# Kernel optimization log

Hardware: AMD Instinct MI355X
Metric: run time of the kernel (lower is better)

## Reference

```python
import jax, jax.numpy as jnp
from jax import lax
import numpy as np

EPS = 1e-5
NH = 16  # attention heads (c // 16 with c = 256)


def _qconv(x, mod, phase, padding=0, groups=1):
    """Quaternion conv: real weight = modulus * cos(phase), applied per quaternion component.
    x: (B, C, Q, H, W) -> (B, O, Q, H, W)"""
    w = mod * jnp.cos(phase)
    B, C, Qd, H, W = x.shape
    xr = jnp.transpose(x, (0, 2, 1, 3, 4)).reshape(B * Qd, C, H, W)
    y = lax.conv_general_dilated(xr, w, (1, 1), [(padding, padding)] * 2,
                                 dimension_numbers=('NCHW', 'OIHW', 'NCHW'),
                                 feature_group_count=groups)
    O, Ho, Wo = y.shape[1], y.shape[2], y.shape[3]
    return jnp.transpose(y.reshape(B, Qd, O, Ho, Wo), (0, 2, 1, 3, 4))


def _bn(x):
    # IQBN/VQBN: per-channel normalization over (batch, quaternion, spatial), no affine
    m = x.mean(axis=(0, 2, 3, 4), keepdims=True)
    v = x.var(axis=(0, 2, 3, 4), keepdims=True)
    return (x - m) * lax.rsqrt(v + EPS)


def _attn(x, qkv_m, qkv_p, aproj_m, aproj_p, pe_m, pe_p):
    # QAttention: per-component multi-head self-attention over spatial tokens
    B, C, Qd, H, W = x.shape
    kd = C // NH
    qkv = _qconv(x, qkv_m, qkv_p)  # (B, 3C, Q, H, W)
    q, k, v = jnp.split(qkv, 3, axis=1)
    q = q.reshape(B, NH, kd, Qd, H * W)
    k = k.reshape(B, NH, kd, Qd, H * W)
    v = v.reshape(B, NH, kd, Qd, H * W)
    scores = jnp.einsum('bhcqn,bhcqm->bhqnm', q, k) * (kd ** -0.5)
    a = jax.nn.softmax(scores, axis=-1)
    out = jnp.einsum('bhqnm,bhdqm->bhdqn', a, v).reshape(B, C, Qd, H, W)
    # proj + depthwise positional conv on the input
    return _qconv(out, aproj_m, aproj_p) + _qconv(x, pe_m, pe_p, padding=1, groups=C)


def _psa(x, qkv_m, qkv_p, aproj_m, aproj_p, pe_m, pe_p, ffn1_m, ffn1_p, ffn2_m, ffn2_p):
    a = _attn(x, qkv_m, qkv_p, aproj_m, aproj_p, pe_m, pe_p) + x  # attn shortcut
    h = jax.nn.relu(_bn(_qconv(a, ffn1_m, ffn1_p)))
    f = _bn(_qconv(h, ffn2_m, ffn2_p))
    return f + a  # ffn shortcut


def _msab(x, guide, ec_m, ec_p, gl_w, gl_b, mproj_m, mproj_p):
    # MaxSigmoidAttnBlock (nh=1): global sigmoid gate per (batch, quaternion component)
    B, C, Qd, H, W = x.shape
    e = jax.nn.relu(_bn(_qconv(x, ec_m, ec_p)))  # (B, ec, Q, H, W)
    g = guide @ gl_w.T + gl_b                     # (B, ec)
    ec = g.shape[-1]
    a = jnp.einsum('bcqhw,bc->bq', e, g) / jnp.sqrt(jnp.asarray(ec * H * W, jnp.float32))
    a = jax.nn.sigmoid(a)  # scale param = 1.0 (scale=False)
    e = e * a[:, None, :, None, None]
    return jax.nn.relu(_bn(_qconv(e, mproj_m, mproj_p, padding=1)))


def _forward(x, guide, cv1_m, cv1_p, qkv_m, qkv_p, aproj_m, aproj_p, pe_m, pe_p,
             ffn1_m, ffn1_p, ffn2_m, ffn2_p, ec_m, ec_p, gl_w, gl_b,
             mproj_m, mproj_p, cv2_m, cv2_p):
    y = jax.nn.relu(_bn(_qconv(x, cv1_m, cv1_p)))       # (B, 2c, Q, H, W)
    a, b = jnp.split(y, 2, axis=1)                       # each (B, c, Q, H, W)
    p = _psa(b, qkv_m, qkv_p, aproj_m, aproj_p, pe_m, pe_p,
             ffn1_m, ffn1_p, ffn2_m, ffn2_p)
    m = _msab(p, guide, ec_m, ec_p, gl_w, gl_b, mproj_m, mproj_p)
    cat = jnp.concatenate([a, b, p, m], axis=1)          # (B, 4c, Q, H, W)
    return jax.nn.relu(_bn(_qconv(cat, cv2_m, cv2_p)))   # (B, c2, Q, H, W)


def setup_inputs():
    B, C1, Qd, H, W = 2, 512, 4, 24, 24
    c = 256; ecd = 128; gc = 512; C2 = 512
    ks = jax.random.split(jax.random.key(0), 24)
    def rp(k, shape, s=0.02):
        return s * jax.random.normal(k, shape, dtype=jnp.float32)
    return {
        'x': jax.random.normal(ks[0], (B, C1, Qd, H, W), dtype=jnp.float32),
        'guide': jax.random.normal(ks[1], (B, gc), dtype=jnp.float32),
        'cv1_m': rp(ks[2], (2 * c, C1, 1, 1)),
        'cv1_p': rp(ks[3], (2 * c, C1, 1, 1), 0.1),
        'qkv_m': rp(ks[4], (3 * c, c, 1, 1)),
        'qkv_p': rp(ks[5], (3 * c, c, 1, 1), 0.1),
        'aproj_m': rp(ks[6], (c, c, 1, 1)),
        'aproj_p': rp(ks[7], (c, c, 1, 1), 0.1),
        'pe_m': rp(ks[8], (c, 1, 3, 3)),
        'pe_p': rp(ks[9], (c, 1, 3, 3), 0.1),
        'ffn1_m': rp(ks[10], (2 * c, c, 1, 1)),
        'ffn1_p': rp(ks[11], (2 * c, c, 1, 1), 0.1),
        'ffn2_m': rp(ks[12], (c, 2 * c, 1, 1)),
        'ffn2_p': rp(ks[13], (c, 2 * c, 1, 1), 0.1),
        'ec_m': rp(ks[14], (ecd, c, 1, 1)),
        'ec_p': rp(ks[15], (ecd, c, 1, 1), 0.1),
        'gl_w': rp(ks[16], (ecd, gc), 0.05),
        'gl_b': jnp.zeros((ecd,), dtype=jnp.float32),
        'mproj_m': rp(ks[17], (c, ecd, 3, 3)),
        'mproj_p': rp(ks[18], (c, ecd, 3, 3), 0.1),
        'cv2_m': rp(ks[19], (C2, 4 * c, 1, 1)),
        'cv2_p': rp(ks[20], (C2, 4 * c, 1, 1), 0.1),
    }


def reference(x, guide, cv1_m, cv1_p, qkv_m, qkv_p, aproj_m, aproj_p, pe_m, pe_p,
              ffn1_m, ffn1_p, ffn2_m, ffn2_p, ec_m, ec_p, gl_w, gl_b,
              mproj_m, mproj_p, cv2_m, cv2_p):
    return _forward(x, guide, cv1_m, cv1_p, qkv_m, qkv_p, aproj_m, aproj_p, pe_m, pe_p,
                    ffn1_m, ffn1_p, ffn2_m, ffn2_p, ec_m, ec_p, gl_w, gl_b,
                    mproj_m, mproj_p, cv2_m, cv2_p)
```

## Files before the change

kernel.cpp:

```cpp
#include <hip/hip_runtime.h>
#include <math.h>

typedef __bf16 bf16x8 __attribute__((ext_vector_type(8)));
typedef float f32x4 __attribute__((ext_vector_type(4)));
typedef unsigned short u16;
typedef unsigned int u32;

__device__ __forceinline__ u16 f2bf(float f) {
  u32 u = __float_as_uint(f);
  u32 r = u + 0x7FFF + ((u >> 16) & 1);
  return (u16)(r >> 16);
}
__device__ __forceinline__ float bf2f(u16 h) { return __uint_as_float(((u32)h) << 16); }

static constexpr size_t OB_WBF = 0;
static constexpr size_t OB_WPE = 3276800;
static constexpr size_t OB_ST  = 3286016;
static constexpr size_t OB_GV  = 3310592;
static constexpr size_t OB_GACC= 3311616;
static constexpr size_t OB_CAT = 3311872;
static constexpr size_t OB_YA  = OB_CAT + 9437184;
static constexpr size_t OB_U1  = OB_YA + 9437184;
static constexpr size_t OB_U2  = OB_U1 + 4718592;
static constexpr size_t OB_U3  = OB_U2 + 14155776;
static constexpr size_t OB_AOB = OB_U3 + 4718592;
static constexpr size_t OB_A1B = OB_AOB + 2359296;
static constexpr size_t WS_TOTAL = OB_A1B + 2359296;

struct HeadP {
  const float* m[8]; const float* p[8]; u16* wout;
  const float* pem; const float* pep; float* peout;
  const float* x; u16* xb;
  const float* guide; const float* glw; const float* glb; float* gv;
  int cum[9]; int nwp;
};
__global__ __launch_bounds__(256) void k_head(HeadP P) {
  int bid = blockIdx.x;
  if (bid < P.nwp) {
    int i = bid * 256 + threadIdx.x;
    if (i < 2304) {
      int tap = i >> 8, c = i & 255;
      P.peout[i] = P.pem[c * 9 + tap] * cosf(P.pep[c * 9 + tap]);
    }
    if (i >= P.cum[8]) return;
    int s = 0;
    while (s < 7 && i >= P.cum[s + 1]) s++;
    int j = i - P.cum[s];
    int src = j;
    if (s == 6) {
      int o = j / 1152, r = j % 1152, kk = r >> 7, cc = r & 127;
      src = (o * 128 + cc) * 9 + kk;
    }
    P.wout[i] = f2bf(P.m[s][src] * cosf(P.p[s][src]));
    return;
  }
  bid -= P.nwp;
  if (bid < 2304) {
    int mt = bid % 18; bid /= 18;
    int ct = bid % 16; bid /= 16;
    int q = bid & 3, b = bid >> 2;
    __shared__ float tile[32][33];
    int tj = threadIdx.x & 31, ti = threadIdx.x >> 5;
    const float* xp = P.x + (((size_t)(b * 512 + ct * 32) * 4 + q) * 576) + mt * 32;
#pragma unroll
    for (int ii = 0; ii < 4; ii++)
      tile[ti + ii * 8][tj] = xp[(size_t)(ti + ii * 8) * 4 * 576 + tj];
    __syncthreads();
    u16* yp = P.xb + ((size_t)b * 2304 + q * 576 + mt * 32) * 512 + ct * 32;
#pragma unroll
    for (int mm = 0; mm < 4; mm++)
      yp[(size_t)(mm * 8 + ti) * 512 + tj] = f2bf(tile[tj][mm * 8 + ti]);
    return;
  }
  bid -= 2304;
  int wv = threadIdx.x >> 6, lane = threadIdx.x & 63;
  int be = bid * 4 + wv;
  int b = be >> 7, e = be & 127;
  const float* gr = P.guide + b * 512;
  const float* wr = P.glw + e * 512;
  float s = 0.f;
  for (int c = lane; c < 512; c += 64) s = fmaf(gr[c], wr[c], s);
#pragma unroll
  for (int off = 32; off > 0; off >>= 1) s += __shfl_down(s, off, 64);
  if (lane == 0) P.gv[be] = s + P.glb[e];
}

struct GemmP {
  const u16* W; const u16* X; float* Y; u16* Yb; float* St;
  const u16* CAT; const float* W9;
  const float* EF; const float* GA;
  long long xOff[8];
  int lda, O, K, M, G;
};

template <int BM, int NWO, int WO, int WM, int MODE>
__global__ __launch_bounds__(256) void k_gemm(GemmP P) {
  constexpr int FO = WO / 16, FM = WM / 16;
  __shared__ __align__(16) char lds[16384 + BM * 128];
  const int mt = P.M / BM;
  const int ot = P.O >> 7;
  int bid = blockIdx.x;
  const int g = bid / (mt * ot);
  const int rr = bid % (mt * ot);
  const int ob = (rr / mt) << 7;
  const int mb = (rr % mt) * BM;
  const int t = threadIdx.x, lane = t & 63, wave = t >> 6;
  const int wo = (wave % NWO) * WO, wm = (wave / NWO) * WM;
  const u16* Wp = P.W + (size_t)ob * P.K;
  const u16* Xp = (MODE == 2) ? nullptr : (P.X + P.xOff[g] + (size_t)mb * P.lda);

  float gt = 0.f;
  int bq2304 = 0;
  if constexpr (MODE == 2) {
    bq2304 = (g >> 2) * 2304 + (g & 3) * 576;
    float a = P.GA[g] / sqrtf(73728.0f);
    gt = 1.f / (1.f + __expf(-a));
  }

  f32x4 acc[FO][FM] = {};

  for (int k0 = 0; k0 < P.K; k0 += 64) {
#pragma unroll
    for (int i = 0; i < 4; i++) {
      int s = (i * 4 + wave) * 64 + lane;
      int row = s >> 3;
      int kg = (s & 7) ^ (row & 7);
      const u16* src = Wp + (size_t)row * P.K + k0 + kg * 8;
      __builtin_amdgcn_global_load_lds(
          (const __attribute__((address_space(1))) u32*)src,
          (__attribute__((address_space(3))) u32*)(lds + (size_t)(i * 4 + wave) * 1024),
          16, 0, 0);
    }
    if constexpr (MODE != 2) {
#pragma unroll
      for (int i = 0; i < BM * 8 / 256; i++) {
        int s = (i * 4 + wave) * 64 + lane;
        int row = s >> 3;
        int kg = (s & 7) ^ (row & 7);
        const u16* src = Xp + (size_t)row * P.lda + k0 + kg * 8;
        __builtin_amdgcn_global_load_lds(
            (const __attribute__((address_space(1))) u32*)src,
            (__attribute__((address_space(3))) u32*)(lds + 16384 + (size_t)(i * 4 + wave) * 1024),
            16, 0, 0);
      }
    } else {
#pragma unroll
      for (int i = 0; i < 2; i++) {
        int s = t + i * 256;
        int row = s >> 3, kg = s & 7;
        int k = k0 + kg * 8;
        int kk = k >> 7, cc = k & 127;
        int n = mb + row;
        int h = n / 24 + kk / 3 - 1, w = n % 24 + kk % 3 - 1;
        u16 pk[8];
        if (h >= 0 && h < 24 && w >= 0 && w < 24) {
          const float* ep = P.EF + ((size_t)(bq2304 + h * 24 + w)) * 128 + cc;
          f32x4 v0 = *(const f32x4*)ep;
          f32x4 v1 = *(const f32x4*)(ep + 4);
#pragma unroll
          for (int j = 0; j < 4; j++) {
            pk[j] = f2bf(v0[j] * gt);
            pk[4 + j] = f2bf(v1[j] * gt);
          }
        } else {
#pragma unroll
          for (int j = 0; j < 8; j++) pk[j] = 0;
        }
        *(uint4*)&lds[16384 + (((row << 3) + (kg ^ (row & 7))) << 4)] = *(uint4*)pk;
      }
    }
    __syncthreads();
#pragma unroll
    for (int kk = 0; kk < 2; kk++) {
      int kgl = kk * 4 + (lane >> 4);
      bf16x8 af[FO], bfm[FM];
#pragma unroll
      for (int fo = 0; fo < FO; fo++) {
        int row = wo + fo * 16 + (lane & 15);
        af[fo] = *(bf16x8*)&lds[((row << 3) + (kgl ^ (row & 7))) << 4];
      }
#pragma unroll
      for (int fm = 0; fm < FM; fm++) {
        int row = wm + fm * 16 + (lane & 15);
        bfm[fm] = *(bf16x8*)&lds[16384 + (((row << 3) + (kgl ^ (row & 7))) << 4)];
      }
#pragma unroll
      for (int fo = 0; fo < FO; fo++)
#pragma unroll
        for (int fm = 0; fm < FM; fm++)
          acc[fo][fm] = __builtin_amdgcn_mfma_f32_16x16x32_bf16(af[fo], bfm[fm], acc[fo][fm], 0, 0, 0);
    }
    __syncthreads();
  }

  size_t ybase = (size_t)g * P.M * P.O;
#pragma unroll
  for (int fo = 0; fo < FO; fo++) {
    int ow = ob + wo + fo * 16 + ((lane >> 4) << 2);
#pragma unroll
    for (int fm = 0; fm < FM; fm++) {
      int m = mb + wm + fm * 16 + (lane & 15);
      f32x4 v = acc[fo][fm];
      if constexpr (MODE == 1) {
        size_t tokc = ((size_t)g * 2304 + m) * 1024 + 256 + ow;
        ushort4 cv = *(const ushort4*)&P.CAT[tokc];
        v[0] += bf2f(cv.x); v[1] += bf2f(cv.y); v[2] += bf2f(cv.z); v[3] += bf2f(cv.w);
        int q_ = m / 576, hw_ = m % 576, h_ = hw_ / 24, w_ = hw_ % 24;
        size_t rowb = ((size_t)g * 2304 + q_ * 576) * 1024 + 256 + ow;
#pragma unroll
        for (int tp = 0; tp < 9; tp++) {
          int hh = h_ + tp / 3 - 1, ww = w_ + tp % 3 - 1;
          if (hh < 0 || hh > 23 || ww < 0 || ww > 23) continue;
          ushort4 tv = *(const ushort4*)&P.CAT[rowb + (size_t)(hh * 24 + ww) * 1024];
          f32x4 wt = *(const f32x4*)&P.W9[tp * 256 + ow];
          v[0] = fmaf(wt[0], bf2f(tv.x), v[0]);
          v[1] = fmaf(wt[1], bf2f(tv.y), v[1]);
          v[2] = fmaf(wt[2], bf2f(tv.z), v[2]);
          v[3] = fmaf(wt[3], bf2f(tv.w), v[3]);
        }
        acc[fo][fm] = v;
      }
      size_t off = ybase + (size_t)m * P.O + ow;
      if (P.Y) *(f32x4*)&P.Y[off] = v;
      if (P.Yb) {
        ushort4 r;
        r.x = f2bf(v[0]); r.y = f2bf(v[1]); r.z = f2bf(v[2]); r.w = f2bf(v[3]);
        *(ushort4*)&P.Yb[off] = r;
      }
    }
  }

  if (P.St) {
#pragma unroll
    for (int fo = 0; fo < FO; fo++) {
      float sv[4], qv[4];
#pragma unroll
      for (int j = 0; j < 4; j++) { sv[j] = 0.f; qv[j] = 0.f; }
#pragma unroll
      for (int fm = 0; fm < FM; fm++)
#pragma unroll
        for (int j = 0; j < 4; j++) {
          float a = acc[fo][fm][j];
          sv[j] += a;
          qv[j] = fmaf(a, a, qv[j]);
        }
#pragma unroll
      for (int j = 0; j < 4; j++) {
#pragma unroll
        for (int mk = 1; mk < 16; mk <<= 1) {
          sv[j] += __shfl_xor(sv[j], mk, 64);
          qv[j] += __shfl_xor(qv[j], mk, 64);
        }
      }
      if ((lane & 15) == 0) {
        int o = ob + wo + fo * 16 + ((lane >> 4) << 2);
#pragma unroll
        for (int j = 0; j < 4; j++) {
          atomicAdd(&P.St[2 * (o + j)], sv[j]);
          atomicAdd(&P.St[2 * (o + j) + 1], qv[j]);
        }
      }
    }
  }
}

struct NormP {
  const float* X; const float* st; const u16* AddB;
  u16* Yb; float* Yf; const float* gv; float* gacc;
  long long ybOff[8];
  int ldyb, O, G, M, relu;
  float n;
};
__global__ __launch_bounds__(256) void k_norm(NormP P) {
  int O4 = P.O >> 2;
  long long idx = (long long)blockIdx.x * 256 + threadIdx.x;
  if (idx >= (long long)P.G * P.M * O4) return;
  int c4 = (int)(idx % O4);
  long long gm = idx / O4;
  int m = (int)(gm % P.M);
  int g = (int)(gm / P.M);
  size_t off = (size_t)gm * P.O + c4 * 4;
  f32x4 v = *(const f32x4*)&P.X[off];
  float inv_n = 1.0f / P.n;
#pragma unroll
  for (int j = 0; j < 4; j++) {
    int c = c4 * 4 + j;
    float mean = P.st[2 * c] * inv_n;
    float var = P.st[2 * c + 1] * inv_n - mean * mean;
    v[j] = (v[j] - mean) * rsqrtf(var + 1e-5f);
  }
  if (P.AddB) {
    ushort4 av = *(const ushort4*)(P.AddB + off);
    v[0] += bf2f(av.x); v[1] += bf2f(av.y); v[2] += bf2f(av.z); v[3] += bf2f(av.w);
  }
  if (P.relu) {
#pragma unroll
    for (int j = 0; j < 4; j++) v[j] = fmaxf(v[j], 0.f);
  }
  if (P.Yb) {
    ushort4 r;
    r.x = f2bf(v[0]); r.y = f2bf(v[1]); r.z = f2bf(v[2]); r.w = f2bf(v[3]);
    *(ushort4*)(P.Yb + P.ybOff[g] + (size_t)m * P.ldyb + c4 * 4) = r;
  }
  if (P.Yf) *(f32x4*)&P.Yf[off] = v;
  if (P.gacc) {
    float gs = 0.f;
#pragma unroll
    for (int j = 0; j < 4; j++) gs = fmaf(v[j], P.gv[g * 128 + c4 * 4 + j], gs);
#pragma unroll
    for (int mk = 1; mk < 64; mk <<= 1) gs += __shfl_xor(gs, mk, 64);
    __shared__ float t1[4];
    int lane = threadIdx.x & 63, wv = threadIdx.x >> 6;
    if (lane == 0) t1[wv] = gs;
    __syncthreads();
    if (threadIdx.x == 0)
      atomicAdd(&P.gacc[g * 4 + m / 576], t1[0] + t1[1] + t1[2] + t1[3]);
  }
}

__global__ __launch_bounds__(256) void k_normT(const float* X, const float* st, float* out) {
  int bid = blockIdx.x;
  int ot = bid & 15;
  int mt = (bid >> 4) % 72;
  int b = bid / 1152;
  int mb = mt * 32, ob = ot * 32;
  __shared__ float tile[32][33];
  int c = threadIdx.x & 31, r = threadIdx.x >> 5;
#pragma unroll
  for (int i = 0; i < 4; i++) {
    int row = r + i * 8;
    tile[row][c] = X[((size_t)b * 2304 + mb + row) * 512 + ob + c];
  }
  __syncthreads();
  float inv_n = 1.0f / 4608.0f;
#pragma unroll
  for (int i = 0; i < 4; i++) {
    int o = ob + r + i * 8;
    float mean = st[2 * o] * inv_n;
    float var = st[2 * o + 1] * inv_n - mean * mean;
    float rs = rsqrtf(var + 1e-5f);
    float v = fmaxf((tile[c][r + i * 8] - mean) * rs, 0.f);
    out[((size_t)(b * 512 + o)) * 2304 + mb + c] = v;
  }
}

__global__ __launch_bounds__(256) void k_attn(const u16* qkv, u16* ao) {
  int bid = blockIdx.x;
  int tq = bid % 3; int u = bid / 3;
  int qd = u & 3; u >>= 2;
  int head = u & 15, b = u >> 4;
  int t = threadIdx.x, lane = t & 63, wv = t >> 6;
  int g = lane >> 4, q = lane & 15;
  size_t tok0 = (size_t)b * 2304 + qd * 576;
  const u16* QKV = qkv + tok0 * 768;

  __shared__ __align__(16) char shm[50176];
  u16* Kl = (u16*)(shm);
  u16* VT = (u16*)(shm + 27648);
  u16* Pl = (u16*)(shm + 46080 + wv * 1024);

  for (int i = t; i < 1152; i += 256) {
    int m = i >> 1, half = i & 1;
    const u16* src = QKV + (size_t)m * 768 + 256 + head * 16 + half * 8;
    u16 tmp[8];
    *(uint4*)tmp = *(const uint4*)src;
    ushort4 lo, hi;
    lo.x = f2bf(bf2f(tmp[0]) * 0.25f); lo.y = f2bf(bf2f(tmp[1]) * 0.25f);
    lo.z = f2bf(bf2f(tmp[2]) * 0.25f); lo.w = f2bf(bf2f(tmp[3]) * 0.25f);
    hi.x = f2bf(bf2f(tmp[4]) * 0.25f); hi.y = f2bf(bf2f(tmp[5]) * 0.25f);
    hi.z = f2bf(bf2f(tmp[6]) * 0.25f); hi.w = f2bf(bf2f(tmp[7]) * 0.25f);
    u16* dst = Kl + m * 24 + half * 8;
    *(ushort4*)dst = lo;
    *(ushort4*)(dst + 4) = hi;
  }
  for (int mm = t; mm < 576; mm += 256) {
    const u16* src = QKV + (size_t)mm * 768 + 512 + head * 16;
    u16 tmp[16];
    *(uint4*)tmp = *(const uint4*)src;
    *(uint4*)(tmp + 8) = *(const uint4*)(src + 8);
    u16* dst = VT + (mm >> 3) * 128 + (mm & 7);
#pragma unroll
    for (int d = 0; d < 16; d++) dst[d * 8] = tmp[d];
  }
  __syncthreads();

#pragma unroll 1
  for (int i = 0; i < 3; i++) {
    int tl = wv * 3 + i;
    int qbase = tq * 192 + tl * 16;
    bf16x8 qf = {};
    if (g < 2)
      qf = *(const bf16x8*)(QKV + (size_t)(qbase + q) * 768 + head * 16 + g * 8);

    f32x4 acc_o = {};
    float ssum = 0.f;

    for (int ch = 0; ch < 18; ch++) {
      int m0 = ch * 32;
      f32x4 s[2];
#pragma unroll
      for (int h = 0; h < 2; h++) {
        bf16x8 kf = {};
        if (g < 2)
          kf = *(const bf16x8*)(Kl + (size_t)(m0 + h * 16 + q) * 24 + g * 8);
        f32x4 z = {};
        s[h] = __builtin_amdgcn_mfma_f32_16x16x32_bf16(kf, qf, z, 0, 0, 0);
      }
#pragma unroll
      for (int h = 0; h < 2; h++) {
        float p0 = __expf(s[h][0]);
        float p1 = __expf(s[h][1]);
        float p2 = __expf(s[h][2]);
        float p3 = __expf(s[h][3]);
        ssum += (p0 + p1) + (p2 + p3);
        ushort4 w;
        w.x = f2bf(p0); w.y = f2bf(p1); w.z = f2bf(p2); w.w = f2bf(p3);
        *(ushort4*)(Pl + ((h * 2 + (g >> 1)) * 16 + q) * 8 + (g & 1) * 4) = w;
      }
      bf16x8 va = *(const bf16x8*)(VT + ((m0 >> 3) + g) * 128 + q * 8);
      bf16x8 pa = *(const bf16x8*)(Pl + (g * 16 + q) * 8);
      acc_o = __builtin_amdgcn_mfma_f32_16x16x32_bf16(va, pa, acc_o, 0, 0, 0);
    }

    ssum += __shfl_xor(ssum, 16, 64);
    ssum += __shfl_xor(ssum, 32, 64);
    float inv = 1.f / ssum;
    u16* op = ao + (tok0 + qbase + q) * 256 + head * 16 + g * 4;
    ushort4 r;
    r.x = f2bf(acc_o[0] * inv);
    r.y = f2bf(acc_o[1] * inv);
    r.z = f2bf(acc_o[2] * inv);
    r.w = f2bf(acc_o[3] * inv);
    *(ushort4*)op = r;
  }
}

extern "C" void kernel_launch(void* const* d_in, const int* in_sizes, int n_in,
                              void* d_out, int out_size, void* d_ws, size_t ws_size,
                              hipStream_t stream) {
  if (ws_size < WS_TOTAL) return;
  char* ws = (char*)d_ws;
  u16* WB = (u16*)(ws + OB_WBF);
  float* WPE = (float*)(ws + OB_WPE);
  float* STB = (float*)(ws + OB_ST);
  float* GV = (float*)(ws + OB_GV);
  float* GACC = (float*)(ws + OB_GACC);
  u16* CATB = (u16*)(ws + OB_CAT);
  float* YA = (float*)(ws + OB_YA);
  u16* XBF = (u16*)(ws + OB_U1);
  u16* QKVB = (u16*)(ws + OB_U2);
  float* EF = (float*)(ws + OB_U2 + 10616832);
  u16* HB = (u16*)(ws + OB_U3);
  u16* AOB = (u16*)(ws + OB_AOB);
  u16* A1B = (u16*)(ws + OB_A1B);
  float* out = (float*)d_out;

  hipMemsetAsync(ws + OB_ST, 0, OB_CAT - OB_ST, stream);

  {
    HeadP p;
    const int mi[8] = {2, 4, 6, 10, 12, 14, 18, 20};
    const int sz[8] = {262144, 196608, 65536, 131072, 131072, 32768, 294912, 524288};
    int c = 0;
    for (int i = 0; i < 8; i++) {
      p.m[i] = (const float*)d_in[mi[i]];
      p.p[i] = (const float*)d_in[mi[i] + 1];
      p.cum[i] = c;
      c += sz[i];
    }
    p.cum[8] = c;
    p.wout = WB;
    p.pem = (const float*)d_in[8];
    p.pep = (const float*)d_in[9];
    p.peout = WPE;
    p.x = (const float*)d_in[0];
    p.xb = XBF;
    p.guide = (const float*)d_in[1];
    p.glw = (const float*)d_in[16];
    p.glb = (const float*)d_in[17];
    p.gv = GV;
    p.nwp = (c + 255) / 256;
    int grid = p.nwp + 2304 + 64;
    k_head<<<grid, 256, 0, stream>>>(p);
  }

  auto gemm = [&](int mode, size_t wOff, int O, int K, int M, int G,
                  const u16* X, long long xs, long long xadd, int lda,
                  float* Y, u16* Yb, int si) {
    GemmP p;
    p.W = WB + wOff; p.X = X; p.Y = Y; p.Yb = Yb;
    p.St = (si >= 0) ? (STB + si * 1024) : nullptr;
    p.CAT = CATB; p.W9 = WPE; p.EF = EF; p.GA = GACC;
    p.lda = lda; p.O = O; p.K = K; p.M = M; p.G = G;
    for (int g = 0; g < 8; g++) p.xOff[g] = (long long)(g < G ? g : 0) * xs + xadd;
    int grid = G * (O / 128) * (M / 64);
    if (mode == 0)
      k_gemm<64, 4, 32, 64, 0><<<grid, 256, 0, stream>>>(p);
    else if (mode == 1)
      k_gemm<64, 4, 32, 64, 1><<<grid, 256, 0, stream>>>(p);
    else
      k_gemm<64, 4, 32, 64, 2><<<grid, 256, 0, stream>>>(p);
  };
  auto norm = [&](const float* X, int si, int O, int G, int M, const u16* AddB,
                  u16* Yb, int ldyb, const long long* ybOff, float* Yf, int relu,
                  const float* gv, float* gacc) {
    NormP p;
    p.X = X; p.st = STB + si * 1024; p.AddB = AddB; p.Yb = Yb; p.Yf = Yf;
    p.gv = gv; p.gacc = gacc;
    p.ldyb = ldyb; p.O = O; p.G = G; p.M = M; p.relu = relu;
    p.n = (float)(G * M);
    for (int g = 0; g < 8; g++) p.ybOff[g] = ybOff ? ybOff[(g < G) ? g : 0] : 0;
    long long total = (long long)G * M * (O / 4);
    k_norm<<<(int)((total + 255) / 256), 256, 0, stream>>>(p);
  };

  gemm(0, 0, 512, 512, 2304, 2, XBF, 2304LL * 512, 0, 512, YA, nullptr, 0);
  { long long yo[2] = {0, 2304LL * 1024};
    norm(YA, 0, 512, 2, 2304, nullptr, CATB, 1024, yo, nullptr, 1, nullptr, nullptr); }

  gemm(0, 262144, 768, 256, 2304, 2, CATB, 2304LL * 1024, 256, 1024, nullptr, QKVB, -1);
  k_attn<<<384, 256, 0, stream>>>(QKVB, AOB);
  gemm(1, 458752, 256, 256, 2304, 2, AOB, 2304LL * 256, 0, 256, nullptr, A1B, -1);

  gemm(0, 524288, 512, 256, 2304, 2, A1B, 2304LL * 256, 0, 256, YA, nullptr, 1);
  { long long yo[2] = {0, 2304LL * 512};
    norm(YA, 1, 512, 2, 2304, nullptr, HB, 512, yo, nullptr, 1, nullptr, nullptr); }

  gemm(0, 655360, 256, 512, 2304, 2, HB, 2304LL * 512, 0, 512, YA, nullptr, 2);
  { long long yo[2] = {512, 2304LL * 1024 + 512};
    norm(YA, 2, 256, 2, 2304, A1B, CATB, 1024, yo, nullptr, 0, nullptr, nullptr); }

  gemm(0, 786432, 128, 256, 2304, 2, CATB, 2304LL * 1024, 512, 1024, YA, nullptr, 3);
  norm(YA, 3, 128, 2, 2304, nullptr, nullptr, 0, nullptr, EF, 1, GV, GACC);

  gemm(2, 819200, 256, 1152, 576, 8, nullptr, 0, 0, 0, YA, nullptr, 4);
  { long long yo[8];
    for (int g = 0; g < 8; g++)
      yo[g] = (long long)(g >> 2) * 2304 * 1024 + (long long)(g & 3) * 576 * 1024 + 768;
    norm(YA, 4, 256, 8, 576, nullptr, CATB, 1024, yo, nullptr, 1, nullptr, nullptr); }

  gemm(0, 1114112, 512, 1024, 2304, 2, CATB, 2304LL * 1024, 0, 1024, YA, nullptr, 5);
  k_normT<<<2304, 256, 0, stream>>>(YA, STB + 5 * 1024, out);
}
```

Baseline: 273.0 us.

## Double-buffer LDS tiles in the GEMM kernel to overlap loads with MFMA

Splits the GEMM k-loop into ping-pong LDS buffers. The next K-tile is issued through global_load_lds, or through register prefetch of the gated EF values in the implicit-conv mode, before the MFMAs on the current tile run. This removes one of the two barriers per iteration and hides global-load latency behind compute. In exchange it doubles LDS use per block, which can lower occupancy, and adds register pressure for the prefetched floats.

```diff
diff --git a/kernel.cpp b/kernel.cpp
--- a/kernel.cpp
+++ b/kernel.cpp
@@ -96,7 +96,8 @@
 template <int BM, int NWO, int WO, int WM, int MODE>
 __global__ __launch_bounds__(256) void k_gemm(GemmP P) {
   constexpr int FO = WO / 16, FM = WM / 16;
-  __shared__ __align__(16) char lds[16384 + BM * 128];
+  constexpr int ABYTES = 16384, BBYTES = BM * 128;
+  __shared__ __align__(16) char lds[2 * ABYTES + 2 * BBYTES];
   const int mt = P.M / BM;
   const int ot = P.O >> 7;
   int bid = blockIdx.x;
@@ -118,8 +119,9 @@
   }
 
   f32x4 acc[FO][FM] = {};
-
-  for (int k0 = 0; k0 < P.K; k0 += 64) {
+  float vreg[2][8];
+
+  auto stageA = [&](int tb, int k0) {
 #pragma unroll
     for (int i = 0; i < 4; i++) {
       int s = (i * 4 + wave) * 64 + lane;
@@ -128,48 +130,78 @@
       const u16* src = Wp + (size_t)row * P.K + k0 + kg * 8;
       __builtin_amdgcn_global_load_lds(
           (const __attribute__((address_space(1))) u32*)src,
-          (__attribute__((address_space(3))) u32*)(lds + (size_t)(i * 4 + wave) * 1024),
+          (__attribute__((address_space(3))) u32*)(lds + tb * ABYTES + (size_t)(i * 4 + wave) * 1024),
           16, 0, 0);
     }
-    if constexpr (MODE != 2) {
-#pragma unroll
-      for (int i = 0; i < BM * 8 / 256; i++) {
-        int s = (i * 4 + wave) * 64 + lane;
-        int row = s >> 3;
-        int kg = (s & 7) ^ (row & 7);
-        const u16* src = Xp + (size_t)row * P.lda + k0 + kg * 8;
-        __builtin_amdgcn_global_load_lds(
-            (const __attribute__((address_space(1))) u32*)src,
-            (__attribute__((address_space(3))) u32*)(lds + 16384 + (size_t)(i * 4 + wave) * 1024),
-            16, 0, 0);
-      }
-    } else {
-#pragma unroll
-      for (int i = 0; i < 2; i++) {
-        int s = t + i * 256;
-        int row = s >> 3, kg = s & 7;
-        int k = k0 + kg * 8;
-        int kk = k >> 7, cc = k & 127;
-        int n = mb + row;
-        int h = n / 24 + kk / 3 - 1, w = n % 24 + kk % 3 - 1;
-        u16 pk[8];
-        if (h >= 0 && h < 24 && w >= 0 && w < 24) {
-          const float* ep = P.EF + ((size_t)(bq2304 + h * 24 + w)) * 128 + cc;
-          f32x4 v0 = *(const f32x4*)ep;
-          f32x4 v1 = *(const f32x4*)(ep + 4);
-#pragma unroll
-          for (int j = 0; j < 4; j++) {
-            pk[j] = f2bf(v0[j] * gt);
-            pk[4 + j] = f2bf(v1[j] * gt);
-          }
-        } else {
-#pragma unroll
-          for (int j = 0; j < 8; j++) pk[j] = 0;
-        }
-        *(uint4*)&lds[16384 + (((row << 3) + (kg ^ (row & 7))) << 4)] = *(uint4*)pk;
-      }
-    }
-    __syncthreads();
+  };
+  auto stageB = [&](int tb, int k0) {
+#pragma unroll
+    for (int i = 0; i < BM * 8 / 256; i++) {
+      int s = (i * 4 + wave) * 64 + lane;
+      int row = s >> 3;
+      int kg = (s & 7) ^ (row & 7);
+      const u16* src = Xp + (size_t)row * P.lda + k0 + kg * 8;
+      __builtin_amdgcn_global_load_lds(
+          (const __attribute__((address_space(1))) u32*)src,
+          (__attribute__((address_space(3))) u32*)(lds + 2 * ABYTES + tb * BBYTES +
+                                                   (size_t)(i * 4 + wave) * 1024),
+          16, 0, 0);
+    }
+  };
+  auto loadEF = [&](int k0) {
+#pragma unroll
+    for (int i = 0; i < 2; i++) {
+      int s = t + i * 256;
+      int row = s >> 3, kg = s & 7;
+      int k = k0 + kg * 8;
+      int kk = k >> 7, cc = k & 127;
+      int n = mb + row;
+      int h = n / 24 + kk / 3 - 1, w = n % 24 + kk % 3 - 1;
+      if (h >= 0 && h < 24 && w >= 0 && w < 24) {
+        const float* ep = P.EF + ((size_t)(bq2304 + h * 24 + w)) * 128 + cc;
+        f32x4 v0 = *(const f32x4*)ep;
+        f32x4 v1 = *(const f32x4*)(ep + 4);
+#pragma unroll
+        for (int j = 0; j < 4; j++) { vreg[i][j] = v0[j]; vreg[i][4 + j] = v1[j]; }
+      } else {
+#pragma unroll
+        for (int j = 0; j < 8; j++) vreg[i][j] = 0.f;
+      }
+    }
+  };
+  auto writeB = [&](int tb) {
+#pragma unroll
+    for (int i = 0; i < 2; i++) {
+      int s = t + i * 256;
+      int row = s >> 3, kg = s & 7;
+      u16 pk[8];
+#pragma unroll
+      for (int j = 0; j < 8; j++) pk[j] = f2bf(vreg[i][j] * gt);
+      *(uint4*)&lds[2 * ABYTES + tb * BBYTES + (((row << 3) + (kg ^ (row & 7))) << 4)] =
+          *(uint4*)pk;
+    }
+  };
+
+  const int nt = P.K >> 6;
+  stageA(0, 0);
+  if constexpr (MODE != 2) {
+    stageB(0, 0);
+  } else {
+    loadEF(0);
+    writeB(0);
+  }
+  __syncthreads();
+
+  for (int tt = 0; tt < nt; tt++) {
+    const int cur = tt & 1, nxt = cur ^ 1;
+    const bool more = (tt + 1) < nt;
+    if (more) {
+      stageA(nxt, (tt + 1) << 6);
+      if constexpr (MODE != 2) stageB(nxt, (tt + 1) << 6);
+      else loadEF((tt + 1) << 6);
+    }
+    const char* bA = lds + cur * ABYTES;
+    const char* bB = lds + 2 * ABYTES + cur * BBYTES;
 #pragma unroll
     for (int kk = 0; kk < 2; kk++) {
       int kgl = kk * 4 + (lane >> 4);
@@ -177,12 +209,12 @@
 #pragma unroll
       for (int fo = 0; fo < FO; fo++) {
         int row = wo + fo * 16 + (lane & 15);
-        af[fo] = *(bf16x8*)&lds[((row << 3) + (kgl ^ (row & 7))) << 4];
+        af[fo] = *(bf16x8*)&bA[((row << 3) + (kgl ^ (row & 7))) << 4];
       }
 #pragma unroll
       for (int fm = 0; fm < FM; fm++) {
         int row = wm + fm * 16 + (lane & 15);
-        bfm[fm] = *(bf16x8*)&lds[16384 + (((row << 3) + (kgl ^ (row & 7))) << 4)];
+        bfm[fm] = *(bf16x8*)&bB[((row << 3) + (kgl ^ (row & 7))) << 4];
       }
 #pragma unroll
       for (int fo = 0; fo < FO; fo++)
@@ -190,7 +222,10 @@
         for (int fm = 0; fm < FM; fm++)
           acc[fo][fm] = __builtin_amdgcn_mfma_f32_16x16x32_bf16(af[fo], bfm[fm], acc[fo][fm], 0, 0, 0);
     }
-    __syncthreads();
+    if (more) {
+      if constexpr (MODE == 2) writeB(nxt);
+      __syncthreads();
+    }
   }
 
   size_t ybase = (size_t)g * P.M * P.O;
```

After: 256.4 us. -6.1%, faster.
